# Optimization experiments

Measured on AMD Instinct MI355X. Metric: run time of the kernel, lower is better.

The kernel has to match this reference:

```python
import jax, jax.numpy as jnp
import numpy as np

DIM = 512
HEADS = 8
HEAD_DIM = DIM // HEADS
WIN = 3
N = WIN * WIN  # 9 tokens per window
HID = 4 * DIM
B = 8192
SCALE = HEAD_DIM ** -0.5
EPS = 1e-5


def _relative_position_index():
    coords = np.stack(np.meshgrid(np.arange(WIN), np.arange(WIN), indexing='ij'))  # (2,W,W)
    flat = coords.reshape(2, -1)  # (2, N)
    rel = flat[:, :, None] - flat[:, None, :]  # (2, N, N)
    rel = rel.transpose(1, 2, 0).copy()  # (N, N, 2)
    rel[:, :, 0] += WIN - 1
    rel[:, :, 1] += WIN - 1
    rel[:, :, 0] *= 2 * WIN - 1
    return rel.sum(-1)  # (N, N) int

REL_IDX = jnp.asarray(_relative_position_index())


def _layernorm(x, g, b):
    mu = jnp.mean(x, axis=-1, keepdims=True)
    var = jnp.mean(jnp.square(x - mu), axis=-1, keepdims=True)
    return (x - mu) * jax.lax.rsqrt(var + EPS) * g + b


def setup_inputs() -> dict:
    key = jax.random.key(0)
    ks = jax.random.split(key, 16)
    f32 = jnp.float32
    return {
        'x': jax.random.normal(ks[0], (B, N, DIM), f32),
        'gamma1': jnp.ones((DIM,), f32),
        'beta1': jnp.zeros((DIM,), f32),
        'w_qkv': jax.random.normal(ks[1], (3 * DIM, DIM), f32) * 0.02,
        'b_qkv': jnp.zeros((3 * DIM,), f32),
        'bias_table': jax.random.normal(ks[2], ((2 * WIN - 1) ** 2, HEADS), f32) * 0.02,
        'w_proj': jax.random.normal(ks[3], (DIM, DIM), f32) * 0.02,
        'b_proj': jnp.zeros((DIM,), f32),
        'gamma2': jnp.ones((DIM,), f32),
        'beta2': jnp.zeros((DIM,), f32),
        'w_fc1': jax.random.normal(ks[4], (HID, DIM), f32) * 0.02,
        'b_fc1': jnp.zeros((HID,), f32),
        'w_fc2': jax.random.normal(ks[5], (DIM, HID), f32) * 0.02,
        'b_fc2': jnp.zeros((DIM,), f32),
        'w_conv': jax.random.normal(ks[6], (DIM, 1, WIN, WIN), f32) * 0.02,
        'b_conv': jnp.zeros((DIM,), f32),
    }


def reference(x, gamma1, beta1, w_qkv, b_qkv, bias_table, w_proj, b_proj,
              gamma2, beta2, w_fc1, b_fc1, w_fc2, b_fc2, w_conv, b_conv):
    Bn, Nn, C = x.shape
    # --- window attention ---
    shortcut = x
    h = _layernorm(x, gamma1, beta1)
    qkv = h @ w_qkv.T + b_qkv  # (B, N, 3C)
    qkv = qkv.reshape(Bn, Nn, 3, HEADS, HEAD_DIM).transpose(2, 0, 3, 1, 4)  # (3,B,H,N,d)
    q, k, v = qkv[0] * SCALE, qkv[1], qkv[2]
    attn = jnp.einsum('bhnd,bhmd->bhnm', q, k)  # (B,H,N,N)
    rel_bias = bias_table[REL_IDX.reshape(-1)].reshape(Nn, Nn, HEADS).transpose(2, 0, 1)  # (H,N,N)
    attn = jax.nn.softmax(attn + rel_bias[None], axis=-1)
    out = jnp.einsum('bhnm,bhmd->bhnd', attn, v)  # (B,H,N,d)
    out = out.transpose(0, 2, 1, 3).reshape(Bn, Nn, C)
    out = out @ w_proj.T + b_proj
    x = shortcut + out
    # --- MLP ---
    h = _layernorm(x, gamma2, beta2)
    h = jax.nn.gelu(h @ w_fc1.T + b_fc1, approximate=False)
    h = h @ w_fc2.T + b_fc2
    x = x + h
    # --- depthwise 3x3 merge conv over the 3x3 grid (valid -> 1x1) ---
    x4 = x.transpose(0, 2, 1).reshape(Bn, C, WIN, WIN)  # (B,C,3,3)
    y = jnp.einsum('bchw,chw->bc', x4, w_conv[:, 0]) + b_conv  # (B,C)
    return y[:, None, :]  # (B,1,C)
```

## Files before the change

### kernel.cpp

```cpp
#include <hip/hip_runtime.h>


typedef short short8 __attribute__((ext_vector_type(8)));
typedef unsigned short ushort8 __attribute__((ext_vector_type(8)));
typedef float floatx4 __attribute__((ext_vector_type(4)));

static constexpr int R_TOT = 73728;

__device__ __forceinline__ unsigned short f2bf(float f) {
  union { float f; unsigned int u; } v; v.f = f;
  unsigned int r = v.u + 0x7FFFu + ((v.u >> 16) & 1u);
  return (unsigned short)(r >> 16);
}
__device__ __forceinline__ float bf2f(unsigned short u) {
  union { unsigned int u; float f; } v; v.u = ((unsigned int)u) << 16;
  return v.f;
}

__device__ __forceinline__ void gload_lds16(const void* g, void* l) {
  __builtin_amdgcn_global_load_lds(
      (const __attribute__((address_space(1))) unsigned int*)g,
      (__attribute__((address_space(3))) unsigned int*)l, 16, 0, 0);
}

#define FENCE asm volatile("" ::: "memory")
#define BAR do { FENCE; __builtin_amdgcn_s_barrier(); FENCE; } while (0)
#define WAITV0 asm volatile("s_waitcnt vmcnt(0)" ::: "memory")
#define WAITV4 asm volatile("s_waitcnt vmcnt(4)" ::: "memory")
#define WAITLG0 asm volatile("s_waitcnt lgkmcnt(0)" ::: "memory")

__global__ __launch_bounds__(256)
void cvt4(const float* __restrict__ in, unsigned short* __restrict__ out) {
  int i = (blockIdx.x * 256 + threadIdx.x) * 4;
  floatx4 v = *(const floatx4*)(in + i);
  union { unsigned short s[4]; unsigned long long u; } pk;
  pk.s[0] = f2bf(v[0]); pk.s[1] = f2bf(v[1]); pk.s[2] = f2bf(v[2]); pk.s[3] = f2bf(v[3]);
  *(unsigned long long*)(out + i) = pk.u;
}

__global__ __launch_bounds__(256)
void ln_bf16(const float* __restrict__ in, const float* __restrict__ g,
             const float* __restrict__ b, unsigned short* __restrict__ out) {
  const int lane = threadIdx.x & 63;
  const int wid = threadIdx.x >> 6;
  const size_t row = (size_t)blockIdx.x * 4 + wid;
  const float* p = in + row * 512 + lane * 8;
  floatx4 v0 = *(const floatx4*)p;
  floatx4 v1 = *(const floatx4*)(p + 4);
  float s = v0[0] + v0[1] + v0[2] + v0[3] + v1[0] + v1[1] + v1[2] + v1[3];
  float ss = v0[0]*v0[0] + v0[1]*v0[1] + v0[2]*v0[2] + v0[3]*v0[3]
           + v1[0]*v1[0] + v1[1]*v1[1] + v1[2]*v1[2] + v1[3]*v1[3];
  #pragma unroll
  for (int m = 1; m < 64; m <<= 1) { s += __shfl_xor(s, m); ss += __shfl_xor(ss, m); }
  float mu = s * (1.f / 512.f);
  float var = ss * (1.f / 512.f) - mu * mu;
  float rs = rsqrtf(var + 1e-5f);
  const float* gp = g + lane * 8;
  const float* bp = b + lane * 8;
  floatx4 g0 = *(const floatx4*)gp, g1 = *(const floatx4*)(gp + 4);
  floatx4 b0 = *(const floatx4*)bp, b1 = *(const floatx4*)(bp + 4);
  ushort8 o;
  o[0] = f2bf((v0[0] - mu) * rs * g0[0] + b0[0]);
  o[1] = f2bf((v0[1] - mu) * rs * g0[1] + b0[1]);
  o[2] = f2bf((v0[2] - mu) * rs * g0[2] + b0[2]);
  o[3] = f2bf((v0[3] - mu) * rs * g0[3] + b0[3]);
  o[4] = f2bf((v1[0] - mu) * rs * g1[0] + b1[0]);
  o[5] = f2bf((v1[1] - mu) * rs * g1[1] + b1[1]);
  o[6] = f2bf((v1[2] - mu) * rs * g1[2] + b1[2]);
  o[7] = f2bf((v1[3] - mu) * rs * g1[3] + b1[3]);
  *(ushort8*)(out + row * 512 + lane * 8) = o;
}


#define STAGE(buf, tk) do { \
  _Pragma("unroll") \
  for (int j = 0; j < 2; ++j) \
    gload_lds16(Ap + (rowB + wid * 32 + j * 16 + sro) * (size_t)K + (tk) + sko, \
                sm + (buf) * 16384 + wid * 2048 + j * 1024); \
  _Pragma("unroll") \
  for (int j = 0; j < 2; ++j) \
    gload_lds16(Wp + (colB + wid * 32 + j * 16 + sro) * (size_t)K + (tk) + sko, \
                sm + (buf) * 16384 + 8192 + wid * 2048 + j * 1024); \
} while (0)

template <int EPI>
__global__ __launch_bounds__(256, 3)
void gemmd(const unsigned short* __restrict__ Ap,
           const unsigned short* __restrict__ Wp,
           const float* __restrict__ bias,
           const float* __restrict__ resid,
           unsigned short* __restrict__ outb,
           float* __restrict__ outf,
           int K, int Nn, int ntn) {
  __shared__ __align__(16) char sm[32768];

  const int t = threadIdx.x;
  const int l = t & 63;
  const int wid = t >> 6;
  const int wm = wid >> 1;
  const int wn = wid & 1;

  const int nwg = gridDim.x;
  const int orig = blockIdx.x;
  const int q8 = nwg >> 3, r8 = nwg & 7;
  const int xcd = orig & 7, idx = orig >> 3;
  const int wg = (xcd < r8 ? xcd * (q8 + 1) : r8 * (q8 + 1) + (xcd - r8) * q8) + idx;
  const int tm = wg / ntn, tn = wg % ntn;
  const size_t rowB = (size_t)tm * 128;
  const size_t colB = (size_t)tn * 128;

  const int sro = l >> 2;
  const int sko = ((l & 3) ^ ((l >> 2) & 3)) * 8;
  const int ro = l & 15;
  const int kx = (((l >> 4) ^ (l & 3)) * 16);

  floatx4 acc[4][4];
  #pragma unroll
  for (int m = 0; m < 4; ++m)
    #pragma unroll
    for (int n = 0; n < 4; ++n)
      acc[m][n] = (floatx4){0.f, 0.f, 0.f, 0.f};

  const int NI = K >> 5;

  STAGE(0, 0);
  STAGE(1, 32);

  for (int kt = 0; kt < NI; ++kt) {
    const int cur = kt & 1;
    if (kt + 1 < NI) { WAITV4; } else { WAITV0; }
    BAR;

    short8 aF[4], bF[4];
    #pragma unroll
    for (int mi = 0; mi < 4; ++mi)
      aF[mi] = *(const short8*)(sm + cur * 16384 + (wm * 64 + mi * 16 + ro) * 64 + kx);
    #pragma unroll
    for (int ni = 0; ni < 4; ++ni)
      bF[ni] = *(const short8*)(sm + cur * 16384 + 8192 + (wn * 64 + ni * 16 + ro) * 64 + kx);
    WAITLG0;
    BAR;

    if (kt + 2 < NI) STAGE(cur, (kt + 2) << 5);

    __builtin_amdgcn_s_setprio(1);
    #pragma unroll
    for (int mi = 0; mi < 4; ++mi)
      #pragma unroll
      for (int ni = 0; ni < 4; ++ni)
        acc[mi][ni] = __builtin_amdgcn_mfma_f32_16x16x32_bf16(aF[mi], bF[ni], acc[mi][ni], 0, 0, 0);
    __builtin_amdgcn_s_setprio(0);
  }
  FENCE;

  #pragma unroll
  for (int mi = 0; mi < 4; ++mi) {
    #pragma unroll
    for (int ni = 0; ni < 4; ++ni) {
      const int rr = (int)rowB + wm * 64 + mi * 16 + (l >> 4) * 4;
      const int cc = (int)colB + wn * 64 + ni * 16 + (l & 15);
      const float bs = bias[cc];
      #pragma unroll
      for (int j = 0; j < 4; ++j) {
        float v = acc[mi][ni][j] + bs;
        if (EPI == 1) v = 0.5f * v * (1.0f + erff(v * 0.70710678118654752f));
        if (EPI == 2) {
          v += resid[(size_t)(rr + j) * Nn + cc];
          outf[(size_t)(rr + j) * Nn + cc] = v;
        } else {
          outb[(size_t)(rr + j) * Nn + cc] = f2bf(v);
        }
      }
    }
  }
}

__global__ __launch_bounds__(256)
void attn9(const unsigned short* __restrict__ qkv,
           const float* __restrict__ bias_table,
           unsigned short* __restrict__ out) {
  __shared__ float qL[4][9][64];
  __shared__ float kL[4][9][64];
  __shared__ float vL[4][9][64];
  __shared__ float sL[4][9][10];

  const int lane = threadIdx.x & 63;
  const int wid = threadIdx.x >> 6;
  const int bh = blockIdx.x * 4 + wid;
  const int b = bh >> 3;
  const int h = bh & 7;

  const size_t base = (size_t)b * 9 * 1536 + h * 64 + lane;
  #pragma unroll
  for (int i = 0; i < 9; ++i) {
    qL[wid][i][lane] = bf2f(qkv[base + i * 1536]) * 0.125f;
    kL[wid][i][lane] = bf2f(qkv[base + i * 1536 + 512]);
    vL[wid][i][lane] = bf2f(qkv[base + i * 1536 + 1024]);
  }
  __syncthreads();

  #pragma unroll
  for (int p = 0; p < 2; ++p) {
    int pair = lane + p * 64;
    if (pair < 81) {
      int i = pair / 9, j = pair % 9;
      const floatx4* qi = (const floatx4*)qL[wid][i];
      const floatx4* kj = (const floatx4*)kL[wid][j];
      float dot = 0.f;
      #pragma unroll
      for (int d = 0; d < 16; ++d) {
        floatx4 a = qi[d], c = kj[d];
        dot += a[0]*c[0] + a[1]*c[1] + a[2]*c[2] + a[3]*c[3];
      }
      int dy = i / 3 - j / 3 + 2;
      int dx = i % 3 - j % 3 + 2;
      dot += bias_table[(dy * 5 + dx) * 8 + h];
      sL[wid][i][j] = dot;
    }
  }
  __syncthreads();

  if (lane < 9) {
    float m = -1e30f;
    #pragma unroll
    for (int j = 0; j < 9; ++j) m = fmaxf(m, sL[wid][lane][j]);
    float e[9], sum = 0.f;
    #pragma unroll
    for (int j = 0; j < 9; ++j) { e[j] = __expf(sL[wid][lane][j] - m); sum += e[j]; }
    float inv = 1.f / sum;
    #pragma unroll
    for (int j = 0; j < 9; ++j) sL[wid][lane][j] = e[j] * inv;
  }
  __syncthreads();

  const size_t obase = (size_t)b * 9 * 512 + h * 64 + lane;
  #pragma unroll
  for (int i = 0; i < 9; ++i) {
    float a = 0.f;
    #pragma unroll
    for (int j = 0; j < 9; ++j) a += sL[wid][i][j] * vL[wid][j][lane];
    out[obase + i * 512] = f2bf(a);
  }
}

__global__ __launch_bounds__(256)
void dwconv9(const float* __restrict__ x2, const float* __restrict__ wc,
             const float* __restrict__ bc, float* __restrict__ out) {
  int idx = blockIdx.x * 256 + threadIdx.x;
  int c = idx & 511;
  int b = idx >> 9;
  const float* xp = x2 + (size_t)b * 9 * 512 + c;
  float acc = bc[c];
  #pragma unroll
  for (int t = 0; t < 9; ++t) acc += xp[t * 512] * wc[c * 9 + t];
  out[idx] = acc;
}

extern "C" void kernel_launch(void* const* d_in, const int* in_sizes, int n_in,
                              void* d_out, int out_size, void* d_ws, size_t ws_size,
                              hipStream_t stream) {
  const float* x      = (const float*)d_in[0];
  const float* gamma1 = (const float*)d_in[1];
  const float* beta1  = (const float*)d_in[2];
  const float* w_qkv  = (const float*)d_in[3];
  const float* b_qkv  = (const float*)d_in[4];
  const float* bias_t = (const float*)d_in[5];
  const float* w_proj = (const float*)d_in[6];
  const float* b_proj = (const float*)d_in[7];
  const float* gamma2 = (const float*)d_in[8];
  const float* beta2  = (const float*)d_in[9];
  const float* w_fc1  = (const float*)d_in[10];
  const float* b_fc1  = (const float*)d_in[11];
  const float* w_fc2  = (const float*)d_in[12];
  const float* b_fc2  = (const float*)d_in[13];
  const float* w_conv = (const float*)d_in[14];
  const float* b_conv = (const float*)d_in[15];
  float* out = (float*)d_out;

  static const int cand[6] = {73728, 36864, 18432, 9216, 4608, 2304};
  int M_C = 2304;
  for (int i = 0; i < 6; ++i) {
    size_t need = 6291456ull + (size_t)cand[i] * 10240ull;
    if (need <= ws_size) { M_C = cand[i]; break; }
  }
  const int nChunks = R_TOT / M_C;
  const int winC = M_C / 9;

  char* ws = (char*)d_ws;
  unsigned short* wqkvb  = (unsigned short*)(ws);
  unsigned short* wprojb = (unsigned short*)(ws + 1572864);
  unsigned short* wfc1b  = (unsigned short*)(ws + 2097152);
  unsigned short* wfc2b  = (unsigned short*)(ws + 4194304);
  char* base = ws + 6291456;
  const size_t szHB  = (size_t)M_C * 1024;
  const size_t szQKV = (size_t)M_C * 3072;
  const size_t szX1  = (size_t)M_C * 2048;
  unsigned short* hb   = (unsigned short*)base;
  unsigned short* aob  = hb;
  unsigned short* qkvb = (unsigned short*)(base + szHB);
  unsigned short* h2b  = qkvb;
  float* x2            = (float*)(base + szHB + szHB);
  float* x1            = (float*)(base + szHB + szQKV);
  unsigned short* gb   = (unsigned short*)(base + szHB + szQKV + szX1);

  cvt4<<<768, 256, 0, stream>>>(w_qkv, wqkvb);
  cvt4<<<256, 256, 0, stream>>>(w_proj, wprojb);
  cvt4<<<1024, 256, 0, stream>>>(w_fc1, wfc1b);
  cvt4<<<1024, 256, 0, stream>>>(w_fc2, wfc2b);

  const int mt128 = M_C / 128;
  for (int ch = 0; ch < nChunks; ++ch) {
    const size_t rOff = (size_t)ch * M_C;
    const float* xC = x + rOff * 512;
    float* outC = out + (size_t)ch * winC * 512;

    ln_bf16<<<M_C / 4, 256, 0, stream>>>(xC, gamma1, beta1, hb);
    gemmd<0><<<dim3(mt128 * 12), 256, 0, stream>>>(hb, wqkvb, b_qkv, nullptr, qkvb, nullptr, 512, 1536, 12);
    attn9<<<winC * 2, 256, 0, stream>>>(qkvb, bias_t, aob);
    gemmd<2><<<dim3(mt128 * 4), 256, 0, stream>>>(aob, wprojb, b_proj, xC, nullptr, x1, 512, 512, 4);
    ln_bf16<<<M_C / 4, 256, 0, stream>>>(x1, gamma2, beta2, h2b);
    gemmd<1><<<dim3(mt128 * 16), 256, 0, stream>>>(h2b, wfc1b, b_fc1, nullptr, gb, nullptr, 512, 2048, 16);
    gemmd<2><<<dim3(mt128 * 4), 256, 0, stream>>>(gb, wfc2b, b_fc2, x1, nullptr, x2, 2048, 512, 4);
    dwconv9<<<winC * 2, 256, 0, stream>>>(x2, w_conv, b_conv, outC);
  }
}
```

Measured before the change: 1.220 ms.

## Vectorize attention and dwconv loads, change GEMM LDS swizzle pattern

The attention kernel now loads q/k/v with 16-byte vector loads (8 bf16 per thread) instead of scalar 2-byte loads. The depthwise conv processes 4 channels per thread with float4 loads and stores, so it launches a quarter of the blocks. The GEMM LDS swizzle XOR terms are changed to use different lane bits, aiming to reduce LDS bank conflicts. The swizzle change must stay consistent between the store and read patterns. The vectorized attention load may also cause LDS write bank conflicts.

```diff
diff --git a/kernel.cpp b/kernel.cpp
--- a/kernel.cpp
+++ b/kernel.cpp
@@ -110,9 +110,9 @@
   const size_t colB = (size_t)tn * 128;
 
   const int sro = l >> 2;
-  const int sko = ((l & 3) ^ ((l >> 2) & 3)) * 8;
+  const int sko = ((l & 3) ^ ((l >> 3) & 3)) * 8;
   const int ro = l & 15;
-  const int kx = (((l >> 4) ^ (l & 3)) * 16);
+  const int kx = (((l >> 4) ^ ((l >> 1) & 3)) * 16);
 
   floatx4 acc[4][4];
   #pragma unroll
@@ -190,12 +190,22 @@
   const int b = bh >> 3;
   const int h = bh & 7;
 
-  const size_t base = (size_t)b * 9 * 1536 + h * 64 + lane;
-  #pragma unroll
-  for (int i = 0; i < 9; ++i) {
-    qL[wid][i][lane] = bf2f(qkv[base + i * 1536]) * 0.125f;
-    kL[wid][i][lane] = bf2f(qkv[base + i * 1536 + 512]);
-    vL[wid][i][lane] = bf2f(qkv[base + i * 1536 + 1024]);
+  const unsigned short* basep = qkv + (size_t)b * 13824 + h * 64;
+  #pragma unroll
+  for (int tt = 0; tt < 4; ++tt) {
+    int s = tt * 64 + lane;
+    if (s < 216) {
+      int tz = s / 72;
+      int rm = s - tz * 72;
+      int r = rm >> 3;
+      int g = rm & 7;
+      ushort8 raw = *(const ushort8*)(basep + r * 1536 + tz * 512 + g * 8);
+      float* dst = (tz == 0) ? &qL[wid][r][g * 8]
+                 : (tz == 1) ? &kL[wid][r][g * 8] : &vL[wid][r][g * 8];
+      float sc = (tz == 0) ? 0.125f : 1.f;
+      #pragma unroll
+      for (int e = 0; e < 8; ++e) dst[e] = bf2f((unsigned short)raw[e]) * sc;
+    }
   }
   __syncthreads();
 
@@ -247,13 +257,17 @@
 void dwconv9(const float* __restrict__ x2, const float* __restrict__ wc,
              const float* __restrict__ bc, float* __restrict__ out) {
   int idx = blockIdx.x * 256 + threadIdx.x;
-  int c = idx & 511;
-  int b = idx >> 9;
-  const float* xp = x2 + (size_t)b * 9 * 512 + c;
-  float acc = bc[c];
-  #pragma unroll
-  for (int t = 0; t < 9; ++t) acc += xp[t * 512] * wc[c * 9 + t];
-  out[idx] = acc;
+  int c4 = idx & 127;
+  int b = idx >> 7;
+  const float* xp = x2 + (size_t)b * 4608 + c4 * 4;
+  floatx4 acc = *(const floatx4*)(bc + c4 * 4);
+  #pragma unroll
+  for (int t = 0; t < 9; ++t) {
+    floatx4 xv = *(const floatx4*)(xp + t * 512);
+    #pragma unroll
+    for (int e = 0; e < 4; ++e) acc[e] += xv[e] * wc[(c4 * 4 + e) * 9 + t];
+  }
+  *(floatx4*)(out + (size_t)b * 512 + c4 * 4) = acc;
 }
 
 extern "C" void kernel_launch(void* const* d_in, const int* in_sizes, int n_in,
@@ -321,6 +335,6 @@
     ln_bf16<<<M_C / 4, 256, 0, stream>>>(x1, gamma2, beta2, h2b);
     gemmd<1><<<dim3(mt128 * 16), 256, 0, stream>>>(h2b, wfc1b, b_fc1, nullptr, gb, nullptr, 512, 2048, 16);
     gemmd<2><<<dim3(mt128 * 4), 256, 0, stream>>>(gb, wfc2b, b_fc2, x1, nullptr, x2, 2048, 512, 4);
-    dwconv9<<<winC * 2, 256, 0, stream>>>(x2, w_conv, b_conv, outC);
-  }
-}
+    dwconv9<<<winC / 2, 256, 0, stream>>>(x2, w_conv, b_conv, outC);
+  }
+}
```

New measurement: 1.218 ms. No clear change (-0.2%).
